# Performance work log

Measured on AMD Instinct MI355X. Metric: run time of the kernel, lower is better.

Reference implementation:

```python
import jax, jax.numpy as jnp
import numpy as np

D = 512; H = 8; DH = D // H; NB = 4; DMLP = 2048; L = 32; ROPE_DIM = 32
SCALE = DH ** -0.25  # scale_exponent = -0.25, applied to both q and k
EPS = 1e-6


def _rms(x, g):
    return x * jax.lax.rsqrt(jnp.mean(x * x, axis=-1, keepdims=True) + EPS) * g


def _rope_tables(T):
    inv = 1.0 / (10000.0 ** (jnp.arange(0, ROPE_DIM, 2, dtype=jnp.float32) / ROPE_DIM))
    ang = jnp.arange(T, dtype=jnp.float32)[:, None] * inv[None, :]  # (T, ROPE_DIM/2)
    return jnp.cos(ang), jnp.sin(ang)


def _apply_rope(x, cos, sin):
    # x: (N, H, T, DH); rotate first ROPE_DIM dims, interleaved pairs
    xr, rest = x[..., :ROPE_DIM], x[..., ROPE_DIM:]
    x1, x2 = xr[..., 0::2], xr[..., 1::2]
    c = cos[None, None]; s = sin[None, None]
    r1 = x1 * c - x2 * s
    r2 = x1 * s + x2 * c
    rot = jnp.stack([r1, r2], axis=-1).reshape(xr.shape)
    return jnp.concatenate([rot, rest], axis=-1)


def _mha(q_in, kv_in, wq, wk, bk, wv, wo, rope=None):
    # q_in: (N, Lq, D), kv_in: (N, Lk, D); k has bias, q/v/o do not
    N, Lq, _ = q_in.shape
    Lk = kv_in.shape[1]
    q = (q_in @ wq).reshape(N, Lq, H, DH).transpose(0, 2, 1, 3)
    k = (kv_in @ wk + bk).reshape(N, Lk, H, DH).transpose(0, 2, 1, 3)
    v = (kv_in @ wv).reshape(N, Lk, H, DH).transpose(0, 2, 1, 3)
    if rope is not None:
        cos, sin = rope
        q = _apply_rope(q, cos, sin)
        k = _apply_rope(k, cos, sin)
    scores = jnp.einsum('nhqd,nhkd->nhqk', q * SCALE, k * SCALE)
    a = jax.nn.softmax(scores, axis=-1)
    o = jnp.einsum('nhqk,nhkd->nhqd', a, v).transpose(0, 2, 1, 3).reshape(N, Lq, D)
    return o @ wo


def _geglu_mlp(x, w1, w2):
    h = x @ w1                       # (..., 2*DMLP)
    a, g = jnp.split(h, 2, axis=-1)
    return (a * jax.nn.gelu(g)) @ w2


def setup_inputs() -> dict:
    key = jax.random.key(0)
    ks = jax.random.split(key, 16)
    w = lambda k, shape: jax.random.normal(k, shape, dtype=jnp.float32) * 0.02
    B, T, C = 8, 128, 64
    return {
        'source': jax.random.normal(ks[0], (B * T, C, D), dtype=jnp.float32),
        'query_latents': jax.random.normal(ks[1], (L, D), dtype=jnp.float32),
        'ca_ln': jnp.ones((NB, 3, D), jnp.float32),
        'ca_wq': w(ks[2], (NB, D, D)), 'ca_wk': w(ks[3], (NB, D, D)),
        'ca_bk': jnp.zeros((NB, D), jnp.float32),
        'ca_wv': w(ks[4], (NB, D, D)), 'ca_wo': w(ks[5], (NB, D, D)),
        'ca_w1': w(ks[6], (NB, D, 2 * DMLP)), 'ca_w2': w(ks[7], (NB, DMLP, D)),
        'ta_ln': jnp.ones((NB, 2, D), jnp.float32),
        'ta_wq': w(ks[8], (NB, D, D)), 'ta_wk': w(ks[9], (NB, D, D)),
        'ta_bk': jnp.zeros((NB, D), jnp.float32),
        'ta_wv': w(ks[10], (NB, D, D)), 'ta_wo': w(ks[11], (NB, D, D)),
        'ta_w1': w(ks[12], (NB, D, 2 * DMLP)), 'ta_w2': w(ks[13], (NB, DMLP, D)),
        'B': B, 'T': T,
    }


def reference(source, query_latents, ca_ln, ca_wq, ca_wk, ca_bk, ca_wv, ca_wo,
              ca_w1, ca_w2, ta_ln, ta_wq, ta_wk, ta_bk, ta_wv, ta_wo, ta_w1,
              ta_w2, B, T):
    BT = source.shape[0]
    rope = _rope_tables(T)
    latents = jnp.broadcast_to(query_latents[None], (BT, L, D))
    for b in range(NB):
        # --- PerceiverResamplerBlock (spatial cross-attn) ---
        l_n = _rms(latents, ca_ln[b, 0])
        s_n = _rms(source, ca_ln[b, 1])
        kv = jnp.concatenate([s_n, l_n], axis=1)  # (BT, C+L, D)
        latents = latents + _mha(l_n, kv, ca_wq[b], ca_wk[b], ca_bk[b], ca_wv[b], ca_wo[b])
        latents = latents + _geglu_mlp(_rms(latents, ca_ln[b, 2]), ca_w1[b], ca_w2[b])
        # --- TemporalAttentionBlock: (B T) L D -> (B L) T D ---
        x = latents.reshape(B, T, L, D).transpose(0, 2, 1, 3).reshape(B * L, T, D)
        x_n = _rms(x, ta_ln[b, 0])
        x = x + _mha(x_n, x_n, ta_wq[b], ta_wk[b], ta_bk[b], ta_wv[b], ta_wo[b], rope=rope)
        x = x + _geglu_mlp(_rms(x, ta_ln[b, 1]), ta_w1[b], ta_w2[b])
        latents = x.reshape(B, L, T, D).transpose(0, 2, 1, 3).reshape(BT, L, D)
    # '(B T) L D -> B T (L D)'
    return latents.reshape(B, T, L * D)
```

## Files before the change

### kernel.cpp

```cpp
#include <hip/hip_runtime.h>
#include <stdint.h>


typedef short    bf16x8 __attribute__((ext_vector_type(8)));
typedef float    f32x4  __attribute__((ext_vector_type(4)));
typedef uint16_t u16;

__device__ __forceinline__ float bf2f(uint32_t u) {
  union { uint32_t i; float f; } x; x.i = u << 16; return x.f;
}
__device__ __forceinline__ u16 f2bf(float f) {
  union { float f; uint32_t i; } x; x.f = f;
  return (u16)((x.i + 0x7fffu + ((x.i >> 16) & 1u)) >> 16);
}
__device__ __forceinline__ float gelu_t(float x) {
  float u = 0.7978845608028654f * (x + 0.044715f * x * x * x);
  float t = 1.f - 2.f / (__expf(2.f * u) + 1.f);
  return 0.5f * x * (1.f + t);
}
template<int RMAP>
__device__ __forceinline__ int maprow(int r) {
  if (RMAP == 0) return r;
  int b = r >> 12, rem = r & 4095;
  return ((b << 7) + (rem & 127)) * 32 + (rem >> 7);
}
__device__ __forceinline__ void glds16(const u16* g, u16* l) {
  __builtin_amdgcn_global_load_lds((const __attribute__((address_space(1))) uint32_t*)(g),
                                   (__attribute__((address_space(3))) uint32_t*)(l),
                                   16, 0, 0);
}

__global__ __launch_bounds__(256) void transpose_cast(const float* __restrict__ src,
                                                      u16* __restrict__ dst,
                                                      int R, int C, size_t zsD) {
  src += (size_t)blockIdx.z * R * C;
  dst += (size_t)blockIdx.z * zsD;
  __shared__ float t[32][33];
  int c0 = blockIdx.x * 32, r0 = blockIdx.y * 32;
  int tx = threadIdx.x & 31, ty = threadIdx.x >> 5;
#pragma unroll
  for (int i = 0; i < 32; i += 8) t[ty + i][tx] = src[(size_t)(r0 + ty + i) * C + c0 + tx];
  __syncthreads();
#pragma unroll
  for (int i = 0; i < 32; i += 8)
    dst[(size_t)(c0 + ty + i) * R + r0 + tx] = f2bf(t[tx][ty + i]);
}

__global__ __launch_bounds__(256) void transpose_w1(const float* __restrict__ src,
                                                    u16* __restrict__ dst) {
  src += (size_t)blockIdx.z * 512 * 4096;
  dst += (size_t)blockIdx.z * 512 * 4096;
  __shared__ float t[32][33];
  int c0 = blockIdx.x * 32, r0 = blockIdx.y * 32;
  int m0 = (c0 >> 8) * 128 + ((c0 >> 6) & 3) * 32 + ((c0 & 32) ? 2048 : 0);
  int tx = threadIdx.x & 31, ty = threadIdx.x >> 5;
#pragma unroll
  for (int i = 0; i < 32; i += 8) t[ty + i][tx] = src[(size_t)(r0 + ty + i) * 4096 + m0 + tx];
  __syncthreads();
#pragma unroll
  for (int i = 0; i < 32; i += 8)
    dst[(size_t)(c0 + ty + i) * 512 + r0 + tx] = f2bf(t[tx][ty + i]);
}

__global__ void rope_init(float* cosT, float* sinT) {
  int idx = blockIdx.x * 256 + threadIdx.x;
  if (idx < 128 * 16) {
    int t = idx >> 4, j = idx & 15;
    float inv = __expf(-logf(10000.f) * (float)j / 16.f);
    float a = (float)t * inv;
    cosT[idx] = cosf(a);
    sinT[idx] = sinf(a);
  }
}

__global__ __launch_bounds__(256) void init_lat(const float* __restrict__ ql,
                                                float* __restrict__ lat) {
  size_t i = (size_t)blockIdx.x * 256 + threadIdx.x;
  int r = (int)(i >> 7), cw = (int)(i & 127);
  int l = r & 31;
  ((float4*)lat)[i] = ((const float4*)ql)[l * 128 + cw];
}

template<int RMAP>
__global__ __launch_bounds__(256) void rms_rows(const float* __restrict__ src,
                                                const float* __restrict__ g,
                                                u16* __restrict__ out) {
  const int wid = threadIdx.x >> 6, lane = threadIdx.x & 63;
  const int row = (blockIdx.x << 2) + wid;
  const int srow = maprow<RMAP>(row);
  const float4* p = (const float4*)(src + (size_t)srow * 512);
  float4 v0 = p[lane * 2], v1 = p[lane * 2 + 1];
  float ss = v0.x * v0.x + v0.y * v0.y + v0.z * v0.z + v0.w * v0.w +
             v1.x * v1.x + v1.y * v1.y + v1.z * v1.z + v1.w * v1.w;
#pragma unroll
  for (int m = 1; m < 64; m <<= 1) ss += __shfl_xor(ss, m);
  const float rs = rsqrtf(ss * (1.f / 512.f) + 1e-6f);
  const float4* gp = (const float4*)g;
  float4 g0 = gp[lane * 2], g1 = gp[lane * 2 + 1];
  u16 rb[8];
  rb[0] = f2bf(v0.x * rs * g0.x); rb[1] = f2bf(v0.y * rs * g0.y);
  rb[2] = f2bf(v0.z * rs * g0.z); rb[3] = f2bf(v0.w * rs * g0.w);
  rb[4] = f2bf(v1.x * rs * g1.x); rb[5] = f2bf(v1.y * rs * g1.y);
  rb[6] = f2bf(v1.z * rs * g1.z); rb[7] = f2bf(v1.w * rs * g1.w);
  *(int4*)(out + (size_t)row * 512 + lane * 8) = *(int4*)rb;
}

template<int EPI, int RMAP, int AMAP>
__global__ __launch_bounds__(512, 2) void gemm256(const u16* __restrict__ A,
                                                  const u16* __restrict__ A2,
                                                  const u16* __restrict__ Bt,
                                                  u16* __restrict__ outH,
                                                  float* __restrict__ latF,
                                                  const float* __restrict__ bias,
                                                  int M, int N, int K, int nb) {
  __shared__ __align__(16) u16 Ab[3][256 * 64];
  __shared__ __align__(16) u16 Bb[2][256 * 64];
  const int tid = threadIdx.x;
  const int nwg = gridDim.x * gridDim.y;
  int bid = blockIdx.y * gridDim.x + blockIdx.x;
  bid = (bid & 7) * (nwg >> 3) + (bid >> 3);
  const int m0 = (bid / gridDim.x) << 8;
  const int n0 = (bid % gridDim.x) << 8;
  const int wid = tid >> 6, lane = tid & 63;
  const int wm = wid >> 2, wn = wid & 3;
  const int lr = lane & 15, lg = lane >> 4;
  const int rx = (lr & 7) << 3;

  auto stageA = [&](int slot, int kt) {
#pragma unroll
    for (int i = 0; i < 4; ++i) {
      const int e = (i * 512 + tid) * 8;
      const int r = e >> 6;
      const int cs = (e & 63) ^ ((r & 7) << 3);
      const u16* src;
      if constexpr (AMAP == 0) {
        src = A + (size_t)(m0 + r) * K + kt * 64 + cs;
      } else {
        const int R = m0 + r;
        const int n_ = R / 96;
        const int j = R - n_ * 96;
        src = (j < 64) ? A  + ((size_t)((nb + n_) * 64 + j)) * 512 + kt * 64 + cs
                       : A2 + ((size_t)((nb + n_) * 32 + (j - 64))) * 512 + kt * 64 + cs;
      }
      glds16(src, &Ab[slot][e]);
    }
  };
  auto stageB = [&](int slot, int kt) {
#pragma unroll
    for (int i = 0; i < 4; ++i) {
      const int e = (i * 512 + tid) * 8;
      const int r = e >> 6;
      const int cs = (e & 63) ^ ((r & 7) << 3);
      glds16(Bt + (size_t)(n0 + r) * K + kt * 64 + cs, &Bb[slot][e]);
    }
  };

  f32x4 acc[8][4];
#pragma unroll
  for (int i = 0; i < 8; ++i)
#pragma unroll
    for (int j = 0; j < 4; ++j) acc[i][j] = (f32x4){0.f, 0.f, 0.f, 0.f};

  stageA(0, 0);
  stageB(0, 0);
  stageA(1, 1);
  asm volatile("s_waitcnt vmcnt(4)" ::: "memory");
  __builtin_amdgcn_s_barrier();
  asm volatile("" ::: "memory");

  const int nkt = K >> 6;
  int sl0 = 0;
  int sl2 = 2;
  for (int kt = 0; kt < nkt; ++kt) {
    const u16* Abase = &Ab[sl0][0];
    const u16* Bbase = &Bb[kt & 1][0];
    bf16x8 bfr[2][4];
#pragma unroll
    for (int p = 0; p < 4; ++p) {
      if (p == 0 && kt + 1 < nkt) stageB((kt + 1) & 1, kt + 1);
      if (p == 1 && kt + 2 < nkt) stageA(sl2, kt + 2);
      if (p == 0) {
#pragma unroll
        for (int ks = 0; ks < 2; ++ks)
#pragma unroll
          for (int in = 0; in < 4; ++in) {
            const int rw = wn * 64 + in * 16 + lr;
            bfr[ks][in] = *(const bf16x8*)&Bbase[rw * 64 + ((ks * 32 + lg * 8) ^ rx)];
          }
      }
      bf16x8 afr[2][2];
#pragma unroll
      for (int d = 0; d < 2; ++d)
#pragma unroll
        for (int ks = 0; ks < 2; ++ks) {
          const int rw = wm * 128 + (p * 2 + d) * 16 + lr;
          afr[d][ks] = *(const bf16x8*)&Abase[rw * 64 + ((ks * 32 + lg * 8) ^ rx)];
        }
      __builtin_amdgcn_s_setprio(1);
#pragma unroll
      for (int d = 0; d < 2; ++d)
#pragma unroll
        for (int in = 0; in < 4; ++in)
#pragma unroll
          for (int ks = 0; ks < 2; ++ks)
            acc[p * 2 + d][in] = __builtin_amdgcn_mfma_f32_16x16x32_bf16(
                afr[d][ks], bfr[ks][in], acc[p * 2 + d][in], 0, 0, 0);
      __builtin_amdgcn_s_setprio(0);
      if (p == 3) {
        if (kt + 1 < nkt) {
          if (kt + 2 < nkt) asm volatile("s_waitcnt vmcnt(4)" ::: "memory");
          else              asm volatile("s_waitcnt vmcnt(0)" ::: "memory");
          __builtin_amdgcn_s_barrier();
          asm volatile("" ::: "memory");
        }
      } else {
        __builtin_amdgcn_s_barrier();
      }
    }
    sl0 = (sl0 == 2) ? 0 : sl0 + 1;
    sl2 = (sl2 == 2) ? 0 : sl2 + 1;
  }

  if constexpr (EPI == 3) {
    const int t128 = n0 >> 1;
#pragma unroll
    for (int im = 0; im < 8; ++im)
#pragma unroll
      for (int in = 0; in < 2; ++in)
#pragma unroll
        for (int j = 0; j < 4; ++j) {
          const int row = m0 + wm * 128 + im * 16 + lg * 4 + j;
          const int hcol = t128 + wn * 32 + in * 16 + lr;
          outH[(size_t)row * 2048 + hcol] = f2bf(acc[im][in][j] * gelu_t(acc[im][in + 2][j]));
        }
  } else if constexpr (EPI == 2) {
#pragma unroll
    for (int im = 0; im < 8; ++im)
#pragma unroll
      for (int in = 0; in < 4; ++in) {
        const int col = n0 + wn * 64 + in * 16 + lr;
#pragma unroll
        for (int j = 0; j < 4; ++j) {
          const int row = m0 + wm * 128 + im * 16 + lg * 4 + j;
          const size_t rr = (size_t)maprow<RMAP>(row) * 512 + col;
          latF[rr] += acc[im][in][j];
        }
      }
  } else {
    float bv4[4];
    if constexpr (EPI == 1) {
#pragma unroll
      for (int in = 0; in < 4; ++in)
        bv4[in] = (n0 < 512) ? bias[n0 + wn * 64 + in * 16 + lr] : 0.f;
    }
#pragma unroll
    for (int im = 0; im < 8; ++im)
#pragma unroll
      for (int in = 0; in < 4; ++in) {
        const int col = n0 + wn * 64 + in * 16 + lr;
#pragma unroll
        for (int j = 0; j < 4; ++j) {
          const int row = m0 + wm * 128 + im * 16 + lg * 4 + j;
          float v = acc[im][in][j];
          if constexpr (EPI == 1) v += bv4[in];
          outH[(size_t)row * N + col] = f2bf(v);
        }
      }
  }
}

__global__ __launch_bounds__(256) void attn_ca(const u16* q,
                                               const u16* __restrict__ kv,
                                               u16* o, int nb) {
  union __align__(16) SM {
    struct { u16 Qs[32][72]; u16 Ks[96][72]; } qk;
    u16 Pb[32][104];
  };
  __shared__ SM sm;
  __shared__ __align__(16) u16 Vt[64][104];
  __shared__ float pmax[2][32];
  __shared__ float psum[2][32];
  const int nl = blockIdx.x, n = nb + nl, h = blockIdx.y, tid = threadIdx.x;

  {
    int r = tid >> 3, c = (tid & 7) * 8;
    *(int4*)&sm.qk.Qs[r][c] = *(const int4*)&q[((size_t)n * 32 + r) * 512 + h * 64 + c];
  }
#pragma unroll
  for (int i = 0; i < 3; ++i) {
    int idx = i * 256 + tid;
    int r = idx >> 3, c = (idx & 7) * 8;
    *(int4*)&sm.qk.Ks[r][c] = *(const int4*)&kv[((size_t)nl * 96 + r) * 1024 + h * 64 + c];
  }
#pragma unroll
  for (int i = 0; i < 3; ++i) {
    int idx = i * 256 + tid;
    int dg = idx / 96, t = idx - dg * 96;
    int4 pv = *(const int4*)&kv[((size_t)nl * 96 + t) * 1024 + 512 + h * 64 + dg * 8];
    const u16* pu = (const u16*)&pv;
#pragma unroll
    for (int e = 0; e < 8; ++e) Vt[dg * 8 + e][t] = pu[e];
  }
  __syncthreads();

  const int wid = tid >> 6, lane = tid & 63, lr = lane & 15, lg = lane >> 4;
  const int m0 = (wid & 1) * 16, wnq = wid >> 1, nbc = wnq * 48;

  f32x4 sa[3];
#pragma unroll
  for (int f = 0; f < 3; ++f) sa[f] = (f32x4){0.f, 0.f, 0.f, 0.f};
#pragma unroll
  for (int ks = 0; ks < 2; ++ks) {
    bf16x8 a = *(const bf16x8*)&sm.qk.Qs[m0 + lr][ks * 32 + lg * 8];
#pragma unroll
    for (int f = 0; f < 3; ++f) {
      bf16x8 bb = *(const bf16x8*)&sm.qk.Ks[nbc + f * 16 + lr][ks * 32 + lg * 8];
      sa[f] = __builtin_amdgcn_mfma_f32_16x16x32_bf16(a, bb, sa[f], 0, 0, 0);
    }
  }

#pragma unroll
  for (int j = 0; j < 4; ++j) {
    float m = fmaxf(fmaxf(sa[0][j], sa[1][j]), sa[2][j]);
    m = fmaxf(m, __shfl_xor(m, 1));
    m = fmaxf(m, __shfl_xor(m, 2));
    m = fmaxf(m, __shfl_xor(m, 4));
    m = fmaxf(m, __shfl_xor(m, 8));
    if (lr == 0) pmax[wnq][m0 + lg * 4 + j] = m;
  }
  __syncthreads();
#pragma unroll
  for (int j = 0; j < 4; ++j) {
    const int row = m0 + lg * 4 + j;
    const float m = fmaxf(pmax[0][row], pmax[1][row]);
    float s = 0.f;
#pragma unroll
    for (int f = 0; f < 3; ++f) {
      float p = __expf(0.125f * (sa[f][j] - m));
      sa[f][j] = p;
      s += p;
    }
    s += __shfl_xor(s, 1); s += __shfl_xor(s, 2); s += __shfl_xor(s, 4); s += __shfl_xor(s, 8);
    if (lr == 0) psum[wnq][row] = s;
  }
#pragma unroll
  for (int f = 0; f < 3; ++f)
#pragma unroll
    for (int j = 0; j < 4; ++j)
      sm.Pb[m0 + lg * 4 + j][nbc + f * 16 + lr] = f2bf(sa[f][j]);
  __syncthreads();

  const int n0d = wnq * 32;
  f32x4 oa[2];
#pragma unroll
  for (int f = 0; f < 2; ++f) oa[f] = (f32x4){0.f, 0.f, 0.f, 0.f};
#pragma unroll
  for (int ks = 0; ks < 3; ++ks) {
    bf16x8 a = *(const bf16x8*)&sm.Pb[m0 + lr][ks * 32 + lg * 8];
#pragma unroll
    for (int f = 0; f < 2; ++f) {
      bf16x8 bb = *(const bf16x8*)&Vt[n0d + f * 16 + lr][ks * 32 + lg * 8];
      oa[f] = __builtin_amdgcn_mfma_f32_16x16x32_bf16(a, bb, oa[f], 0, 0, 0);
    }
  }
#pragma unroll
  for (int j = 0; j < 4; ++j) {
    const int row = m0 + lg * 4 + j;
    const float inv = 1.f / (psum[0][row] + psum[1][row]);
#pragma unroll
    for (int f = 0; f < 2; ++f)
      o[((size_t)n * 32 + row) * 512 + h * 64 + n0d + f * 16 + lr] = f2bf(oa[f][j] * inv);
  }
}

__global__ __launch_bounds__(256) void attn_ta(const u16* q,
                                               const u16* __restrict__ kv,
                                               const float* __restrict__ cosT,
                                               const float* __restrict__ sinT,
                                               u16* o) {
  union __align__(16) SM {
    struct { u16 Qs[128][72]; u16 Ks[128][72]; } qk;
    u16 Pb[128][136];
  };
  __shared__ SM sm;
  __shared__ __align__(16) u16 Vt[64][136];
  __shared__ float pmax[2][128];
  __shared__ float psum[2][128];
  const int n = blockIdx.x, h = blockIdx.y, tid = threadIdx.x;

#pragma unroll
  for (int i = 0; i < 16; ++i) {
    int idx = i * 256 + tid;
    int t = idx >> 5, pr = idx & 31;
    uint32_t uq = *(const uint32_t*)&q[((size_t)n * 128 + t) * 512 + h * 64 + pr * 2];
    uint32_t uk = *(const uint32_t*)&kv[((size_t)n * 128 + t) * 1024 + h * 64 + pr * 2];
    float q1 = bf2f(uq & 0xffff), q2 = bf2f(uq >> 16);
    float k1 = bf2f(uk & 0xffff), k2 = bf2f(uk >> 16);
    if (pr < 16) {
      float c = cosT[t * 16 + pr], s = sinT[t * 16 + pr];
      float a;
      a = q1 * c - q2 * s; q2 = q1 * s + q2 * c; q1 = a;
      a = k1 * c - k2 * s; k2 = k1 * s + k2 * c; k1 = a;
    }
    sm.qk.Qs[t][pr * 2] = f2bf(q1); sm.qk.Qs[t][pr * 2 + 1] = f2bf(q2);
    sm.qk.Ks[t][pr * 2] = f2bf(k1); sm.qk.Ks[t][pr * 2 + 1] = f2bf(k2);
  }
#pragma unroll
  for (int i = 0; i < 4; ++i) {
    int idx = i * 256 + tid;
    int t = idx & 127, d0 = (idx >> 7) * 8;
    int4 pv = *(const int4*)&kv[((size_t)n * 128 + t) * 1024 + 512 + h * 64 + d0];
    const u16* pu = (const u16*)&pv;
#pragma unroll
    for (int e = 0; e < 8; ++e) Vt[d0 + e][t] = pu[e];
  }
  __syncthreads();

  const int wid = tid >> 6, lane = tid & 63, lr = lane & 15, lg = lane >> 4;
  const int wm = wid >> 1, wn = wid & 1;
  const int rbase = wm * 64;

  f32x4 sa[4][4];
#pragma unroll
  for (int i = 0; i < 4; ++i)
#pragma unroll
    for (int j = 0; j < 4; ++j) sa[i][j] = (f32x4){0.f, 0.f, 0.f, 0.f};
#pragma unroll
  for (int ks = 0; ks < 2; ++ks) {
    bf16x8 av[4], bv[4];
#pragma unroll
    for (int im = 0; im < 4; ++im)
      av[im] = *(const bf16x8*)&sm.qk.Qs[rbase + im * 16 + lr][ks * 32 + lg * 8];
#pragma unroll
    for (int in = 0; in < 4; ++in)
      bv[in] = *(const bf16x8*)&sm.qk.Ks[wn * 64 + in * 16 + lr][ks * 32 + lg * 8];
#pragma unroll
    for (int im = 0; im < 4; ++im)
#pragma unroll
      for (int in = 0; in < 4; ++in)
        sa[im][in] = __builtin_amdgcn_mfma_f32_16x16x32_bf16(av[im], bv[in], sa[im][in], 0, 0, 0);
  }

#pragma unroll
  for (int im = 0; im < 4; ++im)
#pragma unroll
    for (int j = 0; j < 4; ++j) {
      float m = fmaxf(fmaxf(sa[im][0][j], sa[im][1][j]), fmaxf(sa[im][2][j], sa[im][3][j]));
      m = fmaxf(m, __shfl_xor(m, 1));
      m = fmaxf(m, __shfl_xor(m, 2));
      m = fmaxf(m, __shfl_xor(m, 4));
      m = fmaxf(m, __shfl_xor(m, 8));
      if (lr == 0) pmax[wn][rbase + im * 16 + lg * 4 + j] = m;
    }
  __syncthreads();
#pragma unroll
  for (int im = 0; im < 4; ++im)
#pragma unroll
    for (int j = 0; j < 4; ++j) {
      const int row = rbase + im * 16 + lg * 4 + j;
      const float m = fmaxf(pmax[0][row], pmax[1][row]);
      float s = 0.f;
#pragma unroll
      for (int in = 0; in < 4; ++in) {
        float p = __expf(0.125f * (sa[im][in][j] - m));
        sa[im][in][j] = p;
        s += p;
      }
      s += __shfl_xor(s, 1); s += __shfl_xor(s, 2); s += __shfl_xor(s, 4); s += __shfl_xor(s, 8);
      if (lr == 0) psum[wn][row] = s;
    }
#pragma unroll
  for (int im = 0; im < 4; ++im)
#pragma unroll
    for (int in = 0; in < 4; ++in)
#pragma unroll
      for (int j = 0; j < 4; ++j)
        sm.Pb[rbase + im * 16 + lg * 4 + j][wn * 64 + in * 16 + lr] = f2bf(sa[im][in][j]);
  __syncthreads();

  f32x4 oa[2][4];
#pragma unroll
  for (int i = 0; i < 2; ++i)
#pragma unroll
    for (int j = 0; j < 4; ++j) oa[i][j] = (f32x4){0.f, 0.f, 0.f, 0.f};
#pragma unroll
  for (int ks = 0; ks < 4; ++ks) {
    bf16x8 av[2], bv[4];
#pragma unroll
    for (int im = 0; im < 2; ++im)
      av[im] = *(const bf16x8*)&sm.Pb[wid * 32 + im * 16 + lr][ks * 32 + lg * 8];
#pragma unroll
    for (int in = 0; in < 4; ++in)
      bv[in] = *(const bf16x8*)&Vt[in * 16 + lr][ks * 32 + lg * 8];
#pragma unroll
    for (int im = 0; im < 2; ++im)
#pragma unroll
      for (int in = 0; in < 4; ++in)
        oa[im][in] = __builtin_amdgcn_mfma_f32_16x16x32_bf16(av[im], bv[in], oa[im][in], 0, 0, 0);
  }
#pragma unroll
  for (int im = 0; im < 2; ++im)
#pragma unroll
    for (int j = 0; j < 4; ++j) {
      const int qi = wid * 32 + im * 16 + lg * 4 + j;
      const float inv = 1.f / (psum[0][qi] + psum[1][qi]);
#pragma unroll
      for (int in = 0; in < 4; ++in)
        o[((size_t)n * 128 + qi) * 512 + h * 64 + in * 16 + lr] = f2bf(oa[im][in][j] * inv);
    }
}

extern "C" void kernel_launch(void* const* d_in, const int* in_sizes, int n_in,
                              void* d_out, int out_size, void* d_ws, size_t ws_size,
                              hipStream_t stream) {
  const float* source = (const float*)d_in[0];
  const float* qlat   = (const float*)d_in[1];
  const float* ca_ln  = (const float*)d_in[2];
  const float* ca_wq  = (const float*)d_in[3];
  const float* ca_wk  = (const float*)d_in[4];
  const float* ca_bk  = (const float*)d_in[5];
  const float* ca_wv  = (const float*)d_in[6];
  const float* ca_wo  = (const float*)d_in[7];
  const float* ca_w1  = (const float*)d_in[8];
  const float* ca_w2  = (const float*)d_in[9];
  const float* ta_ln  = (const float*)d_in[10];
  const float* ta_wq  = (const float*)d_in[11];
  const float* ta_wk  = (const float*)d_in[12];
  const float* ta_bk  = (const float*)d_in[13];
  const float* ta_wv  = (const float*)d_in[14];
  const float* ta_wo  = (const float*)d_in[15];
  const float* ta_w1  = (const float*)d_in[16];
  const float* ta_w2  = (const float*)d_in[17];
  float* lat = (float*)d_out;
  char* ws = (char*)d_ws;
  (void)in_sizes; (void)n_in; (void)out_size;

  if (ws_size < 251674624ull) return;

  const size_t WQ = 512 * 512, W1SZ = (size_t)512 * 4096, W2SZ = (size_t)2048 * 512;
  const size_t O_CA_WQ = 0,
               O_CA_KV = 4 * WQ,
               O_CA_WO = 12 * WQ,
               O_CA_W1 = 16 * WQ,
               O_CA_W2 = O_CA_W1 + 4 * W1SZ,
               O_TA_WQ = O_CA_W2 + 4 * W2SZ,
               O_TA_KV = O_TA_WQ + 4 * WQ,
               O_TA_WO = O_TA_KV + 8 * WQ,
               O_TA_W1 = O_TA_WO + 4 * WQ,
               O_TA_W2 = O_TA_W1 + 4 * W1SZ;

  u16*   W    = (u16*)ws;
  u16*   xn   = (u16*)(ws + 67108864);
  u16*   shat = (u16*)(ws + 100663296);
  u16*   qb   = (u16*)(ws + 167772160);
  u16*   kvb  = (u16*)(ws + 201326592);
  u16*   h2   = shat;
  u16*   takv = shat;
  float* cosT = (float*)(ws + 251658240);
  float* sinT = (float*)(ws + 251666432);

  transpose_cast<<<dim3(16, 16, 4), 256, 0, stream>>>(ca_wq, W + O_CA_WQ, 512, 512, WQ);
  transpose_cast<<<dim3(16, 16, 4), 256, 0, stream>>>(ca_wk, W + O_CA_KV, 512, 512, 2 * WQ);
  transpose_cast<<<dim3(16, 16, 4), 256, 0, stream>>>(ca_wv, W + O_CA_KV + WQ, 512, 512, 2 * WQ);
  transpose_cast<<<dim3(16, 16, 4), 256, 0, stream>>>(ca_wo, W + O_CA_WO, 512, 512, WQ);
  transpose_w1 <<<dim3(128, 16, 4), 256, 0, stream>>>(ca_w1, W + O_CA_W1);
  transpose_cast<<<dim3(16, 64, 4), 256, 0, stream>>>(ca_w2, W + O_CA_W2, 2048, 512, W2SZ);
  transpose_cast<<<dim3(16, 16, 4), 256, 0, stream>>>(ta_wq, W + O_TA_WQ, 512, 512, WQ);
  transpose_cast<<<dim3(16, 16, 4), 256, 0, stream>>>(ta_wk, W + O_TA_KV, 512, 512, 2 * WQ);
  transpose_cast<<<dim3(16, 16, 4), 256, 0, stream>>>(ta_wv, W + O_TA_KV + WQ, 512, 512, 2 * WQ);
  transpose_cast<<<dim3(16, 16, 4), 256, 0, stream>>>(ta_wo, W + O_TA_WO, 512, 512, WQ);
  transpose_w1 <<<dim3(128, 16, 4), 256, 0, stream>>>(ta_w1, W + O_TA_W1);
  transpose_cast<<<dim3(16, 64, 4), 256, 0, stream>>>(ta_w2, W + O_TA_W2, 2048, 512, W2SZ);
  rope_init<<<8, 256, 0, stream>>>(cosT, sinT);
  init_lat<<<16384, 256, 0, stream>>>(qlat, lat);

  for (int b = 0; b < 4; ++b) {
    const u16* wqt   = W + O_CA_WQ + (size_t)b * WQ;
    const u16* wkvt  = W + O_CA_KV + (size_t)b * 2 * WQ;
    const u16* wot   = W + O_CA_WO + (size_t)b * WQ;
    const u16* w1t   = W + O_CA_W1 + (size_t)b * W1SZ;
    const u16* w2t   = W + O_CA_W2 + (size_t)b * W2SZ;
    const u16* twqt  = W + O_TA_WQ + (size_t)b * WQ;
    const u16* twkvt = W + O_TA_KV + (size_t)b * 2 * WQ;
    const u16* twot  = W + O_TA_WO + (size_t)b * WQ;
    const u16* tw1t  = W + O_TA_W1 + (size_t)b * W1SZ;
    const u16* tw2t  = W + O_TA_W2 + (size_t)b * W2SZ;

    rms_rows<0><<<8192, 256, 0, stream>>>(lat, ca_ln + b * 1536, xn);
    rms_rows<0><<<16384, 256, 0, stream>>>(source, ca_ln + b * 1536 + 512, shat);
    gemm256<0, 0, 0><<<dim3(2, 128), 512, 0, stream>>>(xn, nullptr, wqt, qb, nullptr, nullptr, 32768, 512, 512, 0);
    for (int c = 0; c < 4; ++c) {
      gemm256<1, 0, 1><<<dim3(4, 96), 512, 0, stream>>>(shat, xn, wkvt, kvb, nullptr, ca_bk + b * 512, 24576, 1024, 512, c * 256);
      attn_ca<<<dim3(256, 8), 256, 0, stream>>>(qb, kvb, qb, c * 256);
    }
    gemm256<2, 0, 0><<<dim3(2, 128), 512, 0, stream>>>(qb, nullptr, wot, nullptr, lat, nullptr, 32768, 512, 512, 0);
    rms_rows<0><<<8192, 256, 0, stream>>>(lat, ca_ln + b * 1536 + 1024, xn);
    gemm256<3, 0, 0><<<dim3(16, 128), 512, 0, stream>>>(xn, nullptr, w1t, h2, nullptr, nullptr, 32768, 4096, 512, 0);
    gemm256<2, 0, 0><<<dim3(2, 128), 512, 0, stream>>>(h2, nullptr, w2t, nullptr, lat, nullptr, 32768, 512, 2048, 0);

    rms_rows<1><<<8192, 256, 0, stream>>>(lat, ta_ln + b * 1024, xn);
    gemm256<0, 0, 0><<<dim3(2, 128), 512, 0, stream>>>(xn, nullptr, twqt, qb, nullptr, nullptr, 32768, 512, 512, 0);
    gemm256<1, 0, 0><<<dim3(4, 128), 512, 0, stream>>>(xn, nullptr, twkvt, takv, nullptr, ta_bk + b * 512, 32768, 1024, 512, 0);
    attn_ta<<<dim3(256, 8), 256, 0, stream>>>(qb, takv, cosT, sinT, qb);
    gemm256<2, 1, 0><<<dim3(2, 128), 512, 0, stream>>>(qb, nullptr, twot, nullptr, lat, nullptr, 32768, 512, 512, 0);
    rms_rows<1><<<8192, 256, 0, stream>>>(lat, ta_ln + b * 1024 + 512, xn);
    gemm256<3, 0, 0><<<dim3(16, 128), 512, 0, stream>>>(xn, nullptr, tw1t, h2, nullptr, nullptr, 32768, 4096, 512, 0);
    gemm256<2, 1, 0><<<dim3(2, 128), 512, 0, stream>>>(h2, nullptr, tw2t, nullptr, lat, nullptr, 32768, 512, 2048, 0);
  }
}
```

Before: 5.045 ms.

## Double-buffer A fragments and split global-to-LDS staging across GEMM phases

The main GEMM now loads the next phase's A fragments from LDS into a second register buffer while the current phase's MFMAs run. The next k-tile's B fragments and first A fragments are fetched right after the end-of-tile barrier. Global-to-LDS staging for B and A is split into halves spread across the four phases instead of two bursts. The aim is to hide LDS read latency and even out memory issue, at the cost of more live registers, which could lower occupancy or cause spills.

```diff
diff --git a/kernel.cpp b/kernel.cpp
--- a/kernel.cpp
+++ b/kernel.cpp
@@ -126,10 +126,10 @@
   const int lr = lane & 15, lg = lane >> 4;
   const int rx = (lr & 7) << 3;
 
-  auto stageA = [&](int slot, int kt) {
-#pragma unroll
-    for (int i = 0; i < 4; ++i) {
-      const int e = (i * 512 + tid) * 8;
+  auto stageA = [&](int slot, int kt, int h) {
+#pragma unroll
+    for (int i = 0; i < 2; ++i) {
+      const int e = ((h * 2 + i) * 512 + tid) * 8;
       const int r = e >> 6;
       const int cs = (e & 63) ^ ((r & 7) << 3);
       const u16* src;
@@ -145,76 +145,96 @@
       glds16(src, &Ab[slot][e]);
     }
   };
-  auto stageB = [&](int slot, int kt) {
-#pragma unroll
-    for (int i = 0; i < 4; ++i) {
-      const int e = (i * 512 + tid) * 8;
+  auto stageB = [&](int slot, int kt, int h) {
+#pragma unroll
+    for (int i = 0; i < 2; ++i) {
+      const int e = ((h * 2 + i) * 512 + tid) * 8;
       const int r = e >> 6;
       const int cs = (e & 63) ^ ((r & 7) << 3);
       glds16(Bt + (size_t)(n0 + r) * K + kt * 64 + cs, &Bb[slot][e]);
     }
   };
 
+  bf16x8 bfr[2][4];
+  bf16x8 afrA[2][2], afrB_[2][2];
+  auto readAfr = [&](bf16x8 (&dst)[2][2], const u16* Abase, int p) {
+#pragma unroll
+    for (int d = 0; d < 2; ++d)
+#pragma unroll
+      for (int ks = 0; ks < 2; ++ks) {
+        const int rw = wm * 128 + (p * 2 + d) * 16 + lr;
+        dst[d][ks] = *(const bf16x8*)&Abase[rw * 64 + ((ks * 32 + lg * 8) ^ rx)];
+      }
+  };
+  auto readBfr = [&](const u16* Bbase) {
+#pragma unroll
+    for (int ks = 0; ks < 2; ++ks)
+#pragma unroll
+      for (int in = 0; in < 4; ++in) {
+        const int rw = wn * 64 + in * 16 + lr;
+        bfr[ks][in] = *(const bf16x8*)&Bbase[rw * 64 + ((ks * 32 + lg * 8) ^ rx)];
+      }
+  };
+
   f32x4 acc[8][4];
 #pragma unroll
   for (int i = 0; i < 8; ++i)
 #pragma unroll
     for (int j = 0; j < 4; ++j) acc[i][j] = (f32x4){0.f, 0.f, 0.f, 0.f};
 
-  stageA(0, 0);
-  stageB(0, 0);
-  stageA(1, 1);
+  stageA(0, 0, 0); stageA(0, 0, 1);
+  stageB(0, 0, 0); stageB(0, 0, 1);
+  stageA(1, 1, 0); stageA(1, 1, 1);
   asm volatile("s_waitcnt vmcnt(4)" ::: "memory");
   __builtin_amdgcn_s_barrier();
   asm volatile("" ::: "memory");
+  readBfr(&Bb[0][0]);
+  readAfr(afrA, &Ab[0][0], 0);
 
   const int nkt = K >> 6;
   int sl0 = 0;
   int sl2 = 2;
   for (int kt = 0; kt < nkt; ++kt) {
     const u16* Abase = &Ab[sl0][0];
-    const u16* Bbase = &Bb[kt & 1][0];
-    bf16x8 bfr[2][4];
 #pragma unroll
     for (int p = 0; p < 4; ++p) {
-      if (p == 0 && kt + 1 < nkt) stageB((kt + 1) & 1, kt + 1);
-      if (p == 1 && kt + 2 < nkt) stageA(sl2, kt + 2);
-      if (p == 0) {
-#pragma unroll
-        for (int ks = 0; ks < 2; ++ks)
-#pragma unroll
-          for (int in = 0; in < 4; ++in) {
-            const int rw = wn * 64 + in * 16 + lr;
-            bfr[ks][in] = *(const bf16x8*)&Bbase[rw * 64 + ((ks * 32 + lg * 8) ^ rx)];
-          }
-      }
-      bf16x8 afr[2][2];
-#pragma unroll
-      for (int d = 0; d < 2; ++d)
-#pragma unroll
-        for (int ks = 0; ks < 2; ++ks) {
-          const int rw = wm * 128 + (p * 2 + d) * 16 + lr;
-          afr[d][ks] = *(const bf16x8*)&Abase[rw * 64 + ((ks * 32 + lg * 8) ^ rx)];
-        }
+      if (p <= 1 && kt + 1 < nkt) stageB((kt + 1) & 1, kt + 1, p);
+      if (p >= 2 && kt + 2 < nkt) stageA(sl2, kt + 2, p - 2);
+      if (p < 3) {
+        if ((p & 1) == 0) readAfr(afrB_, Abase, p + 1);
+        else              readAfr(afrA,  Abase, p + 1);
+      }
       __builtin_amdgcn_s_setprio(1);
-#pragma unroll
-      for (int d = 0; d < 2; ++d)
-#pragma unroll
-        for (int in = 0; in < 4; ++in)
-#pragma unroll
-          for (int ks = 0; ks < 2; ++ks)
-            acc[p * 2 + d][in] = __builtin_amdgcn_mfma_f32_16x16x32_bf16(
-                afr[d][ks], bfr[ks][in], acc[p * 2 + d][in], 0, 0, 0);
+      if ((p & 1) == 0) {
+#pragma unroll
+        for (int d = 0; d < 2; ++d)
+#pragma unroll
+          for (int in = 0; in < 4; ++in)
+#pragma unroll
+            for (int ks = 0; ks < 2; ++ks)
+              acc[p * 2 + d][in] = __builtin_amdgcn_mfma_f32_16x16x32_bf16(
+                  afrA[d][ks], bfr[ks][in], acc[p * 2 + d][in], 0, 0, 0);
+      } else {
+#pragma unroll
+        for (int d = 0; d < 2; ++d)
+#pragma unroll
+          for (int in = 0; in < 4; ++in)
+#pragma unroll
+            for (int ks = 0; ks < 2; ++ks)
+              acc[p * 2 + d][in] = __builtin_amdgcn_mfma_f32_16x16x32_bf16(
+                  afrB_[d][ks], bfr[ks][in], acc[p * 2 + d][in], 0, 0, 0);
+      }
       __builtin_amdgcn_s_setprio(0);
-      if (p == 3) {
-        if (kt + 1 < nkt) {
-          if (kt + 2 < nkt) asm volatile("s_waitcnt vmcnt(4)" ::: "memory");
-          else              asm volatile("s_waitcnt vmcnt(0)" ::: "memory");
-          __builtin_amdgcn_s_barrier();
-          asm volatile("" ::: "memory");
-        }
-      } else {
+      if (p < 3) {
         __builtin_amdgcn_s_barrier();
+      } else if (kt + 1 < nkt) {
+        if (kt + 2 < nkt) asm volatile("s_waitcnt vmcnt(4)" ::: "memory");
+        else              asm volatile("s_waitcnt vmcnt(0)" ::: "memory");
+        __builtin_amdgcn_s_barrier();
+        asm volatile("" ::: "memory");
+        const int sln = (sl0 == 2) ? 0 : sl0 + 1;
+        readBfr(&Bb[(kt + 1) & 1][0]);
+        readAfr(afrA, &Ab[sln][0], 0);
       }
     }
     sl0 = (sl0 == 2) ? 0 : sl0 + 1;
```

Result: faster. 4.910 ms (-2.7%).
